# Kernel tuning notes

Measured on AMD Instinct MI355X. Metric: run time of the kernel, lower is better.

## Reference

```python
import jax, jax.numpy as jnp
import numpy as np

# ---- system_parameters stand-ins (external module not in source) ----
D1, D2, D3 = 0.1, 1.0, 2.0
SIZE_X, SIZE_D = 5.0, 5.0
POWER_CONVERT = 10.0  # max power for opt_QoS stand-in
B, H, C = 8192, 96, 4
K1, K2 = 256, 256
D_IN = C + 2


def gamma_calculation(Hn):
    idx = np.arange(Hn)
    J = idx[:, None]  # row j
    I = idx[None, :]  # col i (time t)
    off = (D1 / 8.0 * (SIZE_X + SIZE_D) + D2 / 4.0) * (0.25 ** np.clip(I - 1 - J, 0, None))
    q = np.where(I == J, 2.0 * D1 * SIZE_X + D2, np.where(I > J, off, 0.0))
    gamma_list = q.sum(1)
    # Gamma_mat[j, t] = sum_{i>=t} q[j, i] for t >= j, else 0
    gmat = np.cumsum(q[:, ::-1], axis=1)[:, ::-1]
    gmat = np.where(I >= J, gmat, 0.0)
    return gamma_list.astype(np.float32), gmat.astype(np.float32), q.astype(np.float32)


def opt_qos(state, demand, power_max):
    # stand-in for external opt_QoS: action that serves demand and drains state
    # (nominal efficiency 0.8), capped at max power
    return jnp.minimum(jax.nn.relu(state + demand) / 0.8, power_max)


def setup_inputs() -> dict:
    key = jax.random.key(0)
    ks = jax.random.split(key, 9)
    kaiming = lambda k, shape: jax.random.normal(k, shape, jnp.float32) * np.sqrt(2.0 / shape[1])
    return {
        "policy_in_c": jax.random.uniform(ks[0], (B, H, C), jnp.float32) * 5.0,
        "trans_noise": jax.random.uniform(ks[1], (B, H, 1), jnp.float32) * 0.1,
        "demand_noise": jax.random.uniform(ks[2], (B, H, 1), jnp.float32) * 0.1,
        "action_pre": jax.random.uniform(ks[3], (B, 1), jnp.float32),
        "state_pre": jax.random.uniform(ks[4], (B, 1), jnp.float32) * 5.0,
        "Lambda": jnp.array([0.1], jnp.float32),
        "Budget": jnp.array([10.0], jnp.float32),
        "W1": kaiming(ks[5], (K1, D_IN)),
        "b1": jnp.zeros((K1,), jnp.float32),
        "W2": kaiming(ks[6], (K2, K1)),
        "b2": jnp.zeros((K2,), jnp.float32),
        "W3": kaiming(ks[7], (1, K2)),
        "b3": jnp.zeros((1,), jnp.float32),
    }


def reference(policy_in_c, trans_noise, demand_noise, action_pre, state_pre,
              Lambda, Budget, W1, b1, W2, b2, W3, b3):
    Bsz, Hn = policy_in_c.shape[0], policy_in_c.shape[1]
    gl_np, gmat_np, q_np = gamma_calculation(Hn)
    gamma_list = jnp.asarray(gl_np)                       # [H]
    q_cols = jnp.asarray(q_np.T)                          # q_cols[t] = q_mat[:, t]
    g_cols = jnp.asarray(np.concatenate([gmat_np[:, 1:].T,
                                         np.zeros((1, Hn), np.float32)], 0))  # g_cols[t] = Gamma_mat[:, t+1]
    per_step = Lambda * D3 + Budget / Hn                  # [1]
    bgt0 = per_step * jnp.ones((Bsz, 1), jnp.float32)

    def mlp(x):
        h1 = jax.nn.relu(x @ W1.T + b1)
        h2 = jax.nn.relu(h1 @ W2.T + b2)
        return jax.nn.relu(h2 @ W3.T + b3)

    def step(carry, xs):
        action_, state_, bgt, cum_c, dev, ad_prev = carry
        t, feat, noise, noise2, Gamma, q_col, g_col = xs
        a_ml = mlp(jnp.concatenate([feat, action_, state_], -1))
        demand = feat[:, :1]
        a_prior = opt_qos(state_, demand, POWER_CONVERT)
        sign = (a_ml < a_prior).astype(a_ml.dtype) * 2.0 - 1.0
        a_out = a_ml + jax.nn.relu(jnp.abs(a_ml - a_prior) - bgt / Gamma) * sign
        new_state = jnp.minimum(
            jax.nn.relu(state_ * (1.0 - noise2) + demand - (0.8 + noise) * a_out), 15.0)
        # ---- non-final-step branch (dev zero-padded to [B,H] so full matvec == sliced matmul) ----
        c_cost = D1 * new_state ** 2 + D2 * new_state + D3
        ad_new = jnp.abs(a_out - a_prior)
        dev_new = dev.at[:, t].set(ad_new[:, 0])
        cum_d = dev_new @ q_col                            # [B]
        c_prior = jnp.maximum(D3, c_cost - cum_d[:, None])
        cum_c_new = cum_c + (1.0 + Lambda) * c_prior - c_cost
        cum_d_g = dev_new @ g_col                          # [B]
        bgt_if = jnp.maximum(
            jax.nn.relu(bgt + per_step - ad_new * Gamma),
            cum_c_new - cum_d_g[:, None] + Lambda * D3 + (Budget / Hn) * (t + 2.0))
        # final step uses the stale action_diff from the previous iteration (as in source)
        bgt_else = jax.nn.relu(bgt + per_step - ad_prev * Gamma)
        is_last = t == Hn - 1
        bgt_next = jnp.where(is_last, bgt_else, bgt_if)
        cum_c_next = jnp.where(is_last, cum_c, cum_c_new)
        return (a_out, new_state, bgt_next, cum_c_next, dev_new, ad_new), a_out

    xs = (jnp.arange(Hn),
          jnp.transpose(policy_in_c, (1, 0, 2)),
          jnp.transpose(trans_noise, (1, 0, 2)),
          jnp.transpose(demand_noise, (1, 0, 2)),
          gamma_list, q_cols, g_cols)
    carry0 = (action_pre, state_pre, bgt0, jnp.zeros((Bsz, 1), jnp.float32),
              jnp.zeros((Bsz, Hn), jnp.float32), jnp.zeros((Bsz, 1), jnp.float32))
    _, ys = jax.lax.scan(step, carry0, xs)                 # ys: [H, B, 1]
    return jnp.transpose(ys[:, :, 0])                      # [B, H]
```

## Files before the change

### kernel.cpp

```cpp
#include <hip/hip_runtime.h>
#include <stdint.h>
#include <stddef.h>

typedef float    f32x4 __attribute__((ext_vector_type(4)));
typedef float    f32x2 __attribute__((ext_vector_type(2)));
typedef _Float16 f16x4 __attribute__((ext_vector_type(4)));
typedef _Float16 f16x8 __attribute__((ext_vector_type(8)));

#define HH 96
#define RPB 32
#define OCT 136
#define OSTR 100

#define DPP_ADD(v, ctrl) \
    ((v) + __builtin_bit_cast(float, __builtin_amdgcn_update_dpp( \
        0, __builtin_bit_cast(int, (v)), (ctrl), 0xF, 0xF, true)))

struct SState { float A, S, B, C, SS, AD; };

__device__ __forceinline__ float scan_update(
    SState& st, float psum, float dem, f32x2 nz, f32x4 tb,
    float b3s, float lam, float per_step, bool last)
{
    float a_ml   = fmaxf(psum + b3s, 0.0f);
    float a_prior = fminf(fmaxf(st.S + dem, 0.0f) * 1.25f, 10.0f);
    float sgn    = (a_ml < a_prior) ? 1.0f : -1.0f;
    float a_out  = fmaf(fmaxf(fabsf(a_ml - a_prior) - st.B * tb[2], 0.0f), sgn, a_ml);
    float ns     = fminf(fmaxf(st.S * (1.0f - nz[1]) + dem - (0.8f + nz[0]) * a_out, 0.0f), 15.0f);
    float c_cost = fmaf(fmaf(0.1f, ns, 1.0f), ns, 2.0f);
    float ad_new = fabsf(a_out - a_prior);
    float cum_dv = fmaf(2.0f, ad_new, 0.375f * st.SS);
    float c_prior = fmaxf(2.0f, c_cost - cum_dv);
    float cum_c_new = st.C + (1.0f + lam) * c_prior - c_cost;
    float T      = fmaf(0.25f, st.SS, ad_new);
    float cum_dg = tb[0] * T;
    float bgt_if = fmaxf(fmaxf(st.B + per_step - ad_new * tb[1], 0.0f),
                         cum_c_new - cum_dg + tb[3]);
    float bgt_else = fmaxf(st.B + per_step - st.AD * tb[1], 0.0f);
    if (last) { st.B = bgt_else; }
    else      { st.B = bgt_if; st.C = cum_c_new; }
    st.SS = T; st.AD = ad_new; st.A = a_out; st.S = ns;
    return a_out;
}

__device__ __forceinline__ void phaseA(
    _Float16* h1, const f32x4& f, const SState& st,
    const f16x8* w1A, int lq, int h1wbase)
{
    f16x8 xB = {};
    if (lq == 0) {
        xB[0]=(_Float16)f[0]; xB[1]=(_Float16)f[1];
        xB[2]=(_Float16)f[2]; xB[3]=(_Float16)f[3];
        xB[4]=(_Float16)st.A; xB[5]=(_Float16)st.S;
        xB[6]=(_Float16)1.0f;
    }
    #pragma unroll
    for (int tt = 0; tt < 4; ++tt) {
        f32x4 g = {0.f,0.f,0.f,0.f};
        g = __builtin_amdgcn_mfma_f32_16x16x32_f16(w1A[tt], xB, g, 0, 0, 0);
        f16x4 hv;
        #pragma unroll
        for (int r = 0; r < 4; ++r) hv[r] = (_Float16)fmaxf(g[r], 0.0f);
        *(f16x4*)&h1[h1wbase + tt*(2*OCT)] = hv;
    }
}

__launch_bounds__(512, 2)
__global__ void policy_scan_kernel(
    const float* __restrict__ policy,
    const float* __restrict__ noiseT,
    const float* __restrict__ noiseD,
    const float* __restrict__ action_pre,
    const float* __restrict__ state_pre,
    const float* __restrict__ Lambda1,
    const float* __restrict__ Budget1,
    const float* __restrict__ W1,
    const float* __restrict__ b1,
    const float* __restrict__ W2,
    const float* __restrict__ b2,
    const float* __restrict__ W3,
    const float* __restrict__ b3,
    float* __restrict__ out)
{
    __shared__ __attribute__((aligned(16))) _Float16 h1P[32*OCT];
    __shared__ __attribute__((aligned(16))) _Float16 h1Q[32*OCT];
    __shared__ __attribute__((aligned(16))) float    partP[16*4];
    __shared__ __attribute__((aligned(16))) float    partQ[16*4];
    __shared__ __attribute__((aligned(16))) float    tblLDS[HH*4];
    __shared__ __attribute__((aligned(16))) float    outLDS[RPB*OSTR];

    const int tid   = threadIdx.x;
    const int wv    = tid >> 6;
    const int roleQ = (wv >> 2) & 1;
    const int wid4  = wv & 3;
    const int lane  = tid & 63;
    const int l16   = lane & 15;
    const int lq    = lane >> 4;
    const int r0    = blockIdx.x * RPB;
    const int rbase = r0 + roleQ * 16;

    const float lam  = Lambda1[0];
    const float budH = Budget1[0] * (1.0f/96.0f);
    const float b3s  = b3[0];
    const float per_step = lam * 2.0f + budH;
    if (tid < HH) {
        float e  = __builtin_exp2f(-2.0f * (float)(95 - tid));
        float ft = 0.5f * (1.0f - e);
        float G  = 2.0f + ft;
        *(f32x4*)&tblLDS[tid*4] = f32x4{ft, G, 1.0f/G, lam*2.0f + budH*((float)tid + 2.0f)};
    }

    f16x8 bfr[4][8];
    float b2v[4], w3v[4];
    #pragma unroll
    for (int tt = 0; tt < 4; ++tt) {
        const int n = wid4*64 + tt*16 + l16;
        const float* wrow = W2 + (size_t)n * 256;
        #pragma unroll
        for (int kc = 0; kc < 8; ++kc) {
            const int k0 = kc*32 + lq*8;
            f32x4 u0 = *(const f32x4*)(wrow + k0);
            f32x4 u1 = *(const f32x4*)(wrow + k0 + 4);
            f16x8 v;
            v[0]=(_Float16)u0[0]; v[1]=(_Float16)u0[1]; v[2]=(_Float16)u0[2]; v[3]=(_Float16)u0[3];
            v[4]=(_Float16)u1[0]; v[5]=(_Float16)u1[1]; v[6]=(_Float16)u1[2]; v[7]=(_Float16)u1[3];
            bfr[tt][kc] = v;
        }
        b2v[tt] = b2[n];
        w3v[tt] = W3[n];
    }

    f16x8 w1A[4];
    #pragma unroll
    for (int tt = 0; tt < 4; ++tt) {
        f16x8 w = {};
        if (lq == 0) {
            const int nn = wid4*64 + tt*16 + l16;
            #pragma unroll
            for (int j = 0; j < 6; ++j) w[j] = (_Float16)W1[nn*6 + j];
            w[6] = (_Float16)b1[nn];
        }
        w1A[tt] = w;
    }

    const int h1wbase = (wid4*8 + (lq>>1))*OCT + l16*8 + (lq&1)*4;
    const int h1rbase = lq*OCT + l16*8;

    const float* fRow = policy + (size_t)(rbase + l16) * (HH*4);
    const float* tRow = noiseT + (size_t)(rbase + l16) * HH;
    const float* dRow = noiseD + (size_t)(rbase + l16) * HH;

    SState st = { action_pre[rbase + l16], state_pre[rbase + l16],
                  per_step, 0.f, 0.f, 0.f };

    f32x4 fCur  = *(const f32x4*)(fRow);
    f32x2 nzCur = { tRow[0], dRow[0] };
    f32x4 fNxt;
    f32x2 nzNxt;
    float demPrev = 0.f;
    f32x2 nzPrev  = {0.f, 0.f};
    f32x4 tbPrev  = {0.f, 0.f, 0.f, 0.f};

    if (!roleQ) phaseA(h1P, fCur, st, w1A, lq, h1wbase);
    __syncthreads();

    #pragma unroll 1
    for (int t = 0; t < HH; ++t) {
        const int tn = (t < HH-1) ? t+1 : HH-1;
        if (!roleQ) {
            f32x4 acc[4];
            #pragma unroll
            for (int tt = 0; tt < 4; ++tt) acc[tt] = f32x4{b2v[tt],b2v[tt],b2v[tt],b2v[tt]};
            #pragma unroll
            for (int kc = 0; kc < 8; ++kc) {
                f16x8 a = *(const f16x8*)&h1P[h1rbase + kc*(4*OCT)];
                #pragma unroll
                for (int tt = 0; tt < 4; ++tt)
                    acc[tt] = __builtin_amdgcn_mfma_f32_16x16x32_f16(a, bfr[tt][kc], acc[tt], 0, 0, 0);
            }
            fNxt  = *(const f32x4*)(fRow + tn*4);
            nzNxt = f32x2{ tRow[tn], dRow[tn] };
            #pragma unroll
            for (int r = 0; r < 4; ++r) {
                float s0 = fmaf(w3v[0], fmaxf(acc[0][r], 0.0f), w3v[1] * fmaxf(acc[1][r], 0.0f));
                float s1 = fmaf(w3v[2], fmaxf(acc[2][r], 0.0f), w3v[3] * fmaxf(acc[3][r], 0.0f));
                float v = s0 + s1;
                v = DPP_ADD(v, 0xB1); v = DPP_ADD(v, 0x4E);
                v = DPP_ADD(v, 0x124); v = DPP_ADD(v, 0x128);
                if (l16 == 0) partP[(lq*4 + r)*4 + wid4] = v;
            }
        } else {
            const f32x4 tbCur = *(const f32x4*)&tblLDS[t*4];
            if (t > 0) {
                f32x4 q = *(const f32x4*)&partQ[l16*4];
                float psum = (q[0] + q[1]) + (q[2] + q[3]);
                float aQ = scan_update(st, psum, demPrev, nzPrev, tbPrev,
                                       b3s, lam, per_step, false);
                if (wid4 == 0 && lane < 16) outLDS[(16 + lane)*OSTR + (t-1)] = aQ;
            }
            phaseA(h1Q, fCur, st, w1A, lq, h1wbase);
            demPrev = fCur[0]; nzPrev = nzCur; tbPrev = tbCur;
        }
        __syncthreads();

        if (!roleQ) {
            const f32x4 tb = *(const f32x4*)&tblLDS[t*4];
            f32x4 q = *(const f32x4*)&partP[l16*4];
            float psum = (q[0] + q[1]) + (q[2] + q[3]);
            float aP = scan_update(st, psum, fCur[0], nzCur, tb,
                                   b3s, lam, per_step, t == HH-1);
            if (wid4 == 0 && lane < 16) outLDS[lane*OSTR + t] = aP;
            if (t < HH-1) phaseA(h1P, fNxt, st, w1A, lq, h1wbase);
            fCur = fNxt; nzCur = nzNxt;
        } else {
            f32x4 acc[4];
            #pragma unroll
            for (int tt = 0; tt < 4; ++tt) acc[tt] = f32x4{b2v[tt],b2v[tt],b2v[tt],b2v[tt]};
            #pragma unroll
            for (int kc = 0; kc < 8; ++kc) {
                f16x8 a = *(const f16x8*)&h1Q[h1rbase + kc*(4*OCT)];
                #pragma unroll
                for (int tt = 0; tt < 4; ++tt)
                    acc[tt] = __builtin_amdgcn_mfma_f32_16x16x32_f16(a, bfr[tt][kc], acc[tt], 0, 0, 0);
            }
            fNxt  = *(const f32x4*)(fRow + tn*4);
            nzNxt = f32x2{ tRow[tn], dRow[tn] };
            #pragma unroll
            for (int r = 0; r < 4; ++r) {
                float s0 = fmaf(w3v[0], fmaxf(acc[0][r], 0.0f), w3v[1] * fmaxf(acc[1][r], 0.0f));
                float s1 = fmaf(w3v[2], fmaxf(acc[2][r], 0.0f), w3v[3] * fmaxf(acc[3][r], 0.0f));
                float v = s0 + s1;
                v = DPP_ADD(v, 0xB1); v = DPP_ADD(v, 0x4E);
                v = DPP_ADD(v, 0x124); v = DPP_ADD(v, 0x128);
                if (l16 == 0) partQ[(lq*4 + r)*4 + wid4] = v;
            }
            fCur = fNxt; nzCur = nzNxt;
        }
        __syncthreads();
    }

    if (roleQ) {
        f32x4 q = *(const f32x4*)&partQ[l16*4];
        float psum = (q[0] + q[1]) + (q[2] + q[3]);
        float aQ = scan_update(st, psum, demPrev, nzPrev, tbPrev,
                               b3s, lam, per_step, true);
        if (wid4 == 0 && lane < 16) outLDS[(16 + lane)*OSTR + (HH-1)] = aQ;
    }

    __syncthreads();
    float* oslice = out + (size_t)r0 * HH;
    #pragma unroll
    for (int i = 0; i < 3; ++i) {
        int idx = (i*512 + tid) * 2;
        int row = idx / 96, c = idx - row*96;
        f32x2 v = { outLDS[row*OSTR + c], outLDS[row*OSTR + c + 1] };
        *(f32x2*)&oslice[idx] = v;
    }
}

extern "C" void kernel_launch(void* const* d_in, const int* in_sizes, int n_in,
                              void* d_out, int out_size, void* d_ws, size_t ws_size,
                              hipStream_t stream) {
    policy_scan_kernel<<<dim3(8192 / RPB), dim3(512), 0, stream>>>(
        (const float*)d_in[0],
        (const float*)d_in[1],
        (const float*)d_in[2],
        (const float*)d_in[3],
        (const float*)d_in[4],
        (const float*)d_in[5],
        (const float*)d_in[6],
        (const float*)d_in[7],
        (const float*)d_in[8],
        (const float*)d_in[9],
        (const float*)d_in[10],
        (const float*)d_in[11],
        (const float*)d_in[12],
        (float*)d_out);
}
```

Measured before the change: 249.3 us.

## Preload per-block features and noise into LDS before the time scan

Each block now copies its 32 rows of policy features and both noise streams into shared memory, transposed to time-major, with coalesced loads at kernel start. The per-step strided global loads and the register carries for previous and next values are dropped, and the scan reads from LDS instead. This adds about 74 KB of LDS per block, so the launch-bounds occupancy hint drops from 2 to 1 block per CU. The aim is to remove global-latency stalls from the serial loop, at the cost of less latency hiding across blocks.

```diff
diff --git a/kernel.cpp b/kernel.cpp
--- a/kernel.cpp
+++ b/kernel.cpp
@@ -10,6 +10,7 @@
 #define HH 96
 #define RPB 32
 #define OCT 136
+#define NSTR 64
 #define OSTR 100
 
 #define DPP_ADD(v, ctrl) \
@@ -65,7 +66,7 @@
     }
 }
 
-__launch_bounds__(512, 2)
+__launch_bounds__(512, 1)
 __global__ void policy_scan_kernel(
     const float* __restrict__ policy,
     const float* __restrict__ noiseT,
@@ -82,6 +83,8 @@
     const float* __restrict__ b3,
     float* __restrict__ out)
 {
+    __shared__ __attribute__((aligned(16))) float    featLDS[HH*RPB*4];
+    __shared__ __attribute__((aligned(16))) float    noiseTD[HH*NSTR];
     __shared__ __attribute__((aligned(16))) _Float16 h1P[32*OCT];
     __shared__ __attribute__((aligned(16))) _Float16 h1Q[32*OCT];
     __shared__ __attribute__((aligned(16))) float    partP[16*4];
@@ -97,8 +100,27 @@
     const int l16   = lane & 15;
     const int lq    = lane >> 4;
     const int r0    = blockIdx.x * RPB;
+    const int rloc  = roleQ * 16 + l16;
     const int rbase = r0 + roleQ * 16;
 
+    {
+        const f32x4* src = (const f32x4*)(policy + (size_t)r0 * HH * 4);
+        #pragma unroll
+        for (int i = 0; i < 6; ++i) {
+            int idx = i*512 + tid;
+            int row = idx / 96, t = idx - row*96;
+            *(f32x4*)&featLDS[(t*RPB + row)*4] = src[idx];
+        }
+        const float* s1 = noiseT + (size_t)r0 * HH;
+        const float* s2 = noiseD + (size_t)r0 * HH;
+        #pragma unroll
+        for (int i = 0; i < 6; ++i) {
+            int idx = i*512 + tid;
+            int row = idx / 96, t = idx - row*96;
+            noiseTD[t*NSTR + row*2    ] = s1[idx];
+            noiseTD[t*NSTR + row*2 + 1] = s2[idx];
+        }
+    }
     const float lam  = Lambda1[0];
     const float budH = Budget1[0] * (1.0f/96.0f);
     const float b3s  = b3[0];
@@ -146,27 +168,19 @@
     const int h1wbase = (wid4*8 + (lq>>1))*OCT + l16*8 + (lq&1)*4;
     const int h1rbase = lq*OCT + l16*8;
 
-    const float* fRow = policy + (size_t)(rbase + l16) * (HH*4);
-    const float* tRow = noiseT + (size_t)(rbase + l16) * HH;
-    const float* dRow = noiseD + (size_t)(rbase + l16) * HH;
-
     SState st = { action_pre[rbase + l16], state_pre[rbase + l16],
                   per_step, 0.f, 0.f, 0.f };
 
-    f32x4 fCur  = *(const f32x4*)(fRow);
-    f32x2 nzCur = { tRow[0], dRow[0] };
-    f32x4 fNxt;
-    f32x2 nzNxt;
-    float demPrev = 0.f;
-    f32x2 nzPrev  = {0.f, 0.f};
-    f32x4 tbPrev  = {0.f, 0.f, 0.f, 0.f};
-
-    if (!roleQ) phaseA(h1P, fCur, st, w1A, lq, h1wbase);
+    __syncthreads();
+
+    if (!roleQ) {
+        f32x4 f0 = *(const f32x4*)&featLDS[(0*RPB + rloc)*4];
+        phaseA(h1P, f0, st, w1A, lq, h1wbase);
+    }
     __syncthreads();
 
     #pragma unroll 1
     for (int t = 0; t < HH; ++t) {
-        const int tn = (t < HH-1) ? t+1 : HH-1;
         if (!roleQ) {
             f32x4 acc[4];
             #pragma unroll
@@ -178,8 +192,6 @@
                 for (int tt = 0; tt < 4; ++tt)
                     acc[tt] = __builtin_amdgcn_mfma_f32_16x16x32_f16(a, bfr[tt][kc], acc[tt], 0, 0, 0);
             }
-            fNxt  = *(const f32x4*)(fRow + tn*4);
-            nzNxt = f32x2{ tRow[tn], dRow[tn] };
             #pragma unroll
             for (int r = 0; r < 4; ++r) {
                 float s0 = fmaf(w3v[0], fmaxf(acc[0][r], 0.0f), w3v[1] * fmaxf(acc[1][r], 0.0f));
@@ -190,28 +202,34 @@
                 if (l16 == 0) partP[(lq*4 + r)*4 + wid4] = v;
             }
         } else {
-            const f32x4 tbCur = *(const f32x4*)&tblLDS[t*4];
             if (t > 0) {
-                f32x4 q = *(const f32x4*)&partQ[l16*4];
+                f32x4 q  = *(const f32x4*)&partQ[l16*4];
+                f32x4 tb = *(const f32x4*)&tblLDS[(t-1)*4];
+                f32x2 nz = *(const f32x2*)&noiseTD[(t-1)*NSTR + rloc*2];
+                float dem = featLDS[((t-1)*RPB + rloc)*4];
                 float psum = (q[0] + q[1]) + (q[2] + q[3]);
-                float aQ = scan_update(st, psum, demPrev, nzPrev, tbPrev,
+                float aQ = scan_update(st, psum, dem, nz, tb,
                                        b3s, lam, per_step, false);
                 if (wid4 == 0 && lane < 16) outLDS[(16 + lane)*OSTR + (t-1)] = aQ;
             }
-            phaseA(h1Q, fCur, st, w1A, lq, h1wbase);
-            demPrev = fCur[0]; nzPrev = nzCur; tbPrev = tbCur;
+            f32x4 fq = *(const f32x4*)&featLDS[(t*RPB + rloc)*4];
+            phaseA(h1Q, fq, st, w1A, lq, h1wbase);
         }
         __syncthreads();
 
         if (!roleQ) {
-            const f32x4 tb = *(const f32x4*)&tblLDS[t*4];
-            f32x4 q = *(const f32x4*)&partP[l16*4];
+            f32x4 q  = *(const f32x4*)&partP[l16*4];
+            f32x4 tb = *(const f32x4*)&tblLDS[t*4];
+            f32x2 nz = *(const f32x2*)&noiseTD[t*NSTR + rloc*2];
+            float dem = featLDS[(t*RPB + rloc)*4];
             float psum = (q[0] + q[1]) + (q[2] + q[3]);
-            float aP = scan_update(st, psum, fCur[0], nzCur, tb,
+            float aP = scan_update(st, psum, dem, nz, tb,
                                    b3s, lam, per_step, t == HH-1);
             if (wid4 == 0 && lane < 16) outLDS[lane*OSTR + t] = aP;
-            if (t < HH-1) phaseA(h1P, fNxt, st, w1A, lq, h1wbase);
-            fCur = fNxt; nzCur = nzNxt;
+            if (t < HH-1) {
+                f32x4 fn = *(const f32x4*)&featLDS[((t+1)*RPB + rloc)*4];
+                phaseA(h1P, fn, st, w1A, lq, h1wbase);
+            }
         } else {
             f32x4 acc[4];
             #pragma unroll
@@ -223,8 +241,6 @@
                 for (int tt = 0; tt < 4; ++tt)
                     acc[tt] = __builtin_amdgcn_mfma_f32_16x16x32_f16(a, bfr[tt][kc], acc[tt], 0, 0, 0);
             }
-            fNxt  = *(const f32x4*)(fRow + tn*4);
-            nzNxt = f32x2{ tRow[tn], dRow[tn] };
             #pragma unroll
             for (int r = 0; r < 4; ++r) {
                 float s0 = fmaf(w3v[0], fmaxf(acc[0][r], 0.0f), w3v[1] * fmaxf(acc[1][r], 0.0f));
@@ -234,15 +250,17 @@
                 v = DPP_ADD(v, 0x124); v = DPP_ADD(v, 0x128);
                 if (l16 == 0) partQ[(lq*4 + r)*4 + wid4] = v;
             }
-            fCur = fNxt; nzCur = nzNxt;
         }
         __syncthreads();
     }
 
     if (roleQ) {
-        f32x4 q = *(const f32x4*)&partQ[l16*4];
+        f32x4 q  = *(const f32x4*)&partQ[l16*4];
+        f32x4 tb = *(const f32x4*)&tblLDS[(HH-1)*4];
+        f32x2 nz = *(const f32x2*)&noiseTD[(HH-1)*NSTR + rloc*2];
+        float dem = featLDS[((HH-1)*RPB + rloc)*4];
         float psum = (q[0] + q[1]) + (q[2] + q[3]);
-        float aQ = scan_update(st, psum, demPrev, nzPrev, tbPrev,
+        float aQ = scan_update(st, psum, dem, nz, tb,
                                b3s, lam, per_step, true);
         if (wid4 == 0 && lane < 16) outLDS[(16 + lane)*OSTR + (HH-1)] = aQ;
     }
```

New measurement: 240.6 us. -3.5%, faster.
